# Performance work log

Hardware: AMD Instinct MI355X
Metric: run time of the kernel (lower is better)

Reference implementation:

```python
import math
import jax, jax.numpy as jnp
import numpy as np

H = 2048      # hidden_size
NH = 16       # num_attention_heads
QL = 1536     # q_lora_rank
KVL = 512     # kv_lora_rank
NOPE = 128    # qk_nope_head_dim
ROPE = 64     # qk_rope_head_dim
VD = 128      # v_head_dim
QKH = NOPE + ROPE
B, S = 2, 2048
EPS = 1e-6
MIN_VAL = -1e15


def _rms_norm(x, w, eps=EPS):
    var = jnp.mean(x * x, axis=-1, keepdims=True)
    return w * (x * jax.lax.rsqrt(var + eps))


def _rotate_half(x):
    x1, x2 = jnp.split(x, 2, axis=-1)
    return jnp.concatenate((-x2, x1), axis=-1)


def _rope_tables(seq_len, dim):
    inv_freq = 1.0 / (10000.0 ** (np.arange(0, dim, 2, dtype=np.float32) / dim))
    t = np.arange(seq_len, dtype=np.float32)[:, None]
    freqs = t @ inv_freq[None, :]
    freqs = np.concatenate((freqs, freqs), axis=-1)  # [S, dim]
    return jnp.asarray(np.cos(freqs)), jnp.asarray(np.sin(freqs))


def setup_inputs() -> dict:
    key = jax.random.key(0)
    ks = jax.random.split(key, 16)
    s = 0.02
    inp = {
        "x": jax.random.normal(ks[0], (B, S, H), dtype=jnp.float32),
        "mask": jnp.ones((B, S), dtype=jnp.int32),
        "wq_a_w": jax.random.normal(ks[1], (QL, H), dtype=jnp.float32) * s,
        "wq_a_b": jnp.zeros((QL,), dtype=jnp.float32),
        "q_norm_w": jnp.ones((QL,), dtype=jnp.float32),
        "wq_b_w": jax.random.normal(ks[2], (NH * QKH, QL), dtype=jnp.float32) * s,
        "wq_b_b": jnp.zeros((NH * QKH,), dtype=jnp.float32),
        "wkv_a_w": jax.random.normal(ks[3], (KVL + ROPE, H), dtype=jnp.float32) * s,
        "wkv_a_b": jnp.zeros((KVL + ROPE,), dtype=jnp.float32),
        "kv_norm_w": jnp.ones((KVL,), dtype=jnp.float32),
        "wkv_b_w": jax.random.normal(ks[4], (NH * (NOPE + VD), KVL), dtype=jnp.float32) * s,
        "wo_w": jax.random.normal(ks[5], (H, NH * VD), dtype=jnp.float32) * s,
        "wo_b": jnp.zeros((H,), dtype=jnp.float32),
    }
    return inp


def reference(x, mask, wq_a_w, wq_a_b, q_norm_w, wq_b_w, wq_b_b,
              wkv_a_w, wkv_a_b, kv_norm_w, wkv_b_w, wo_w, wo_b):
    bs, seq, _ = x.shape
    # ---- low-rank Q path ----
    q = x @ wq_a_w.T + wq_a_b                 # [b,s,QL]
    q = _rms_norm(q, q_norm_w)
    q = q @ wq_b_w.T + wq_b_b                 # [b,s,NH*QKH]
    q = q.reshape(bs, seq, NH, QKH)
    q_nope, q_pe = q[..., :NOPE], q[..., NOPE:]
    # ---- low-rank KV path ----
    kv_full = x @ wkv_a_w.T + wkv_a_b          # [b,s,KVL+ROPE]
    kv, k_pe = kv_full[..., :KVL], kv_full[..., KVL:]
    kv = _rms_norm(kv, kv_norm_w)              # latent kv cache [b,s,KVL]
    # ---- RoPE on the small rope slice only ----
    cos, sin = _rope_tables(seq, ROPE)         # [s,ROPE]
    cos_q, sin_q = cos[None, :, None, :], sin[None, :, None, :]
    q_pe = q_pe * cos_q + _rotate_half(q_pe) * sin_q            # [b,s,NH,ROPE]
    k_pe = k_pe * cos[None, :, :] + _rotate_half(k_pe) * sin[None, :, :]  # [b,s,ROPE]
    # ---- weight absorption ----
    wkv_b = wkv_b_w.reshape(NH, NOPE + VD, KVL)
    q_lat = jnp.einsum('bshd,hdc->bshc', q_nope, wkv_b[:, :NOPE])  # absorb W_UK
    scores = (jnp.einsum('bshc,btc->bsht', q_lat, kv)
              + jnp.einsum('bshr,btr->bsht', q_pe, k_pe)) / math.sqrt(QKH)
    # ---- causal + padding mask ----
    causal = jnp.triu(jnp.full((seq, seq), MIN_VAL, dtype=scores.dtype), k=1)
    m = jnp.where(mask[:, None, :] == 0, MIN_VAL, causal[None])    # [b,s,t]
    scores = scores + m[:, :, None, :]
    attn = jax.nn.softmax(scores, axis=-1)                         # [b,s,h,t]
    out = jnp.einsum('bsht,btc->bshc', attn, kv)                   # latent values
    out = jnp.einsum('bshc,hdc->bshd', out, wkv_b[:, NOPE:])       # absorb W_UV
    out = out.reshape(bs, seq, NH * VD) @ wo_w.T + wo_b
    return out
```

## Files before the change

kernel.cpp:

```cpp
#include <hip/hip_runtime.h>
#include <hip/hip_bf16.h>

#define BB   2
#define SS   2048
#define HH   2048
#define NHH  16
#define QLL  1536
#define KVLL 512
#define NOPE_D 128
#define ROPE_D 64
#define QKH_D  192
#define VD_D   128
#define MROWS  (BB*SS)

typedef __attribute__((ext_vector_type(8))) short bf16x8;
typedef __attribute__((ext_vector_type(4))) float f32x4;

__device__ inline float bf2f(unsigned short u) {
    union { float f; unsigned int i; } v; v.i = ((unsigned int)u) << 16; return v.f;
}
__device__ inline unsigned short f2bf(float f) {
    union { float f; unsigned int u; } v; v.f = f;
    unsigned int r = v.u + 0x7fffu + ((v.u >> 16) & 1u);
    return (unsigned short)(r >> 16);
}

__device__ __forceinline__ void gload_lds16(const ushort* g, ushort* l)
{
    __builtin_amdgcn_global_load_lds(
        (const __attribute__((address_space(1))) void*)(g),
        (__attribute__((address_space(3))) void*)(l), 16, 0, 0);
}

__global__ void conv_bf(const float* __restrict__ in, ushort* __restrict__ out, int n4)
{
    int i = blockIdx.x * 256 + threadIdx.x;
    int stride = gridDim.x * 256;
    for (; i < n4; i += stride) {
        float4 v = ((const float4*)in)[i];
        ushort4 u;
        u.x = f2bf(v.x); u.y = f2bf(v.y); u.z = f2bf(v.z); u.w = f2bf(v.w);
        ((ushort4*)out)[i] = u;
    }
}

template<typename TC>
__launch_bounds__(256, 3)
__global__ void gemm_bf(const ushort* __restrict__ A, int lda, size_t Ab, size_t Ah,
                        const ushort* __restrict__ B, int ldb, size_t Bb, size_t Bh,
                        const float* __restrict__ bias,
                        TC* __restrict__ C, int ldc, size_t Cb, size_t Ch,
                        int M, int N, int K)
{
    __shared__ ushort As[128 * 64];
    __shared__ ushort Bs[128 * 64];
    const int z = blockIdx.z, bz = z >> 4, hz = z & 15;
    A += (size_t)bz * Ab + (size_t)hz * Ah;
    B += (size_t)bz * Bb + (size_t)hz * Bh;
    C += (size_t)bz * Cb + (size_t)hz * Ch;
    const int m0 = blockIdx.y * 128, n0 = blockIdx.x * 128;
    const int tid = threadIdx.x, w = tid >> 6, lane = tid & 63;
    const int l15 = lane & 15, q = lane >> 4;
    const int r7 = lane >> 3, c7 = lane & 7;
    const int xork = l15 & 7;

    f32x4 acc[4][4];
#pragma unroll
    for (int i = 0; i < 4; i++)
#pragma unroll
        for (int j = 0; j < 4; j++) acc[i][j] = (f32x4){0.f, 0.f, 0.f, 0.f};

    const int mrow = 64 * (w & 1) + l15;
    const int nrow = 64 * (w >> 1) + l15;

    for (int k0 = 0; k0 < K; k0 += 64) {
#pragma unroll
        for (int i = 0; i < 4; i++) {
            int g = 4 * w + i;
            int row = g * 8 + r7;
            int ch = c7 ^ r7;
            gload_lds16(A + (size_t)(m0 + row) * lda + k0 + ch * 8,
                        As + g * 512 + lane * 8);
            int rb = n0 + row; if (rb > N - 1) rb = N - 1;
            gload_lds16(B + (size_t)rb * ldb + k0 + ch * 8,
                        Bs + g * 512 + lane * 8);
        }
        __syncthreads();
#pragma unroll
        for (int ks = 0; ks < 2; ks++) {
            bf16x8 af[4], bf[4];
            const int ch = ks * 4 + q, chx = ch ^ xork;
#pragma unroll
            for (int mt = 0; mt < 4; mt++)
                af[mt] = *(const bf16x8*)(As + (mrow + 16 * mt) * 64 + chx * 8);
#pragma unroll
            for (int nt = 0; nt < 4; nt++)
                bf[nt] = *(const bf16x8*)(Bs + (nrow + 16 * nt) * 64 + chx * 8);
#pragma unroll
            for (int mt = 0; mt < 4; mt++)
#pragma unroll
                for (int nt = 0; nt < 4; nt++)
                    acc[mt][nt] = __builtin_amdgcn_mfma_f32_16x16x32_bf16(af[mt], bf[nt], acc[mt][nt], 0, 0, 0);
        }
        __syncthreads();
    }

#pragma unroll
    for (int nt = 0; nt < 4; nt++) {
        int n = n0 + nrow + 16 * nt;
        if (n >= N) continue;
        float bv = bias ? bias[n] : 0.f;
#pragma unroll
        for (int mt = 0; mt < 4; mt++) {
#pragma unroll
            for (int r = 0; r < 4; r++) {
                int m = m0 + 64 * (w & 1) + 16 * mt + 4 * q + r;
                float v = acc[mt][nt][r] + bv;
                if constexpr (sizeof(TC) == 2) C[(size_t)m * ldc + n] = f2bf(v);
                else                           C[(size_t)m * ldc + n] = v;
            }
        }
    }
}

__launch_bounds__(256)
__global__ void rmsnorm_bf(const float* __restrict__ x, const float* __restrict__ w,
                           ushort* __restrict__ o, int width)
{
    const float* xr = x + (size_t)blockIdx.x * width;
    ushort* orow = o + (size_t)blockIdx.x * width;
    float ss = 0.f;
    for (int i = threadIdx.x; i < width; i += 256) { float v = xr[i]; ss += v * v; }
    __shared__ float red[256];
    red[threadIdx.x] = ss; __syncthreads();
    for (int off = 128; off > 0; off >>= 1) {
        if (threadIdx.x < off) red[threadIdx.x] += red[threadIdx.x + off];
        __syncthreads();
    }
    float r = rsqrtf(red[0] / (float)width + 1e-6f);
    for (int i = threadIdx.x; i < width; i += 256)
        orow[i] = f2bf(w[i] * xr[i] * r);
}

__device__ inline float rope_val(float xj, float xo, int j, int s)
{
    int i = j & 31;
    float freq = powf(10000.f, -(float)i / 32.f);
    float a = (float)s * freq;
    float sn, cs; sincosf(a, &sn, &cs);
    float other = (j < 32) ? -xo : xo;
    return xj * cs + other * sn;
}

__launch_bounds__(256)
__global__ void finalize_kv(const float* __restrict__ kvf, const float* __restrict__ w,
                            ushort* __restrict__ kvbf)
{
    int m = blockIdx.x, s = m & (SS - 1);
    const float* xr = kvf + (size_t)m * 576;
    float ss = 0.f;
    for (int i = threadIdx.x; i < 512; i += 256) { float v = xr[i]; ss += v * v; }
    __shared__ float red[256];
    red[threadIdx.x] = ss; __syncthreads();
    for (int off = 128; off > 0; off >>= 1) {
        if (threadIdx.x < off) red[threadIdx.x] += red[threadIdx.x + off];
        __syncthreads();
    }
    float r = rsqrtf(red[0] / 512.f + 1e-6f);
    for (int i = threadIdx.x; i < 512; i += 256)
        kvbf[(size_t)m * 576 + i] = f2bf(w[i] * xr[i] * r);
    if (threadIdx.x < 64) {
        int j = threadIdx.x;
        float xj = xr[512 + j], xo = xr[512 + (j ^ 32)];
        kvbf[(size_t)m * 576 + 512 + j] = f2bf(rope_val(xj, xo, j, s));
    }
}

__global__ void rope_q_kernel(ushort* __restrict__ qbuf)
{
    int m = blockIdx.x, s = m & (SS - 1);
    int w = threadIdx.x >> 6, j = threadIdx.x & 63;
    int h = blockIdx.y * 4 + w;
    ushort* p = qbuf + (size_t)m * 3072 + h * QKH_D + NOPE_D;
    float xj = bf2f(p[j]);
    float xo = bf2f(p[j ^ 32]);
    p[j] = f2bf(rope_val(xj, xo, j, s));
}

__global__ void copy_kpe(const ushort* __restrict__ kvbf, ushort* __restrict__ Kf)
{
    int m = blockIdx.x, b = m >> 11, t = m & (SS - 1);
    int j = threadIdx.x & 63;
    ushort v = kvbf[(size_t)m * 576 + 512 + j];
    for (int h = threadIdx.x >> 6; h < NHH; h += 4)
        Kf[((size_t)(b * NHH + h) * SS + t) * QKH_D + NOPE_D + j] = v;
}

#define SCL  0.10411760f
#define PTL  72
#define NJOB 45

__constant__ unsigned char JQT[NJOB] = {18,17,16,19,20,21,22,23,24,25,26,27,28,29,30,31,15,31,14,30,13,29,12,28,11,27,10,26,9,25,8,24,7,23,6,22,5,21,4,20,3,19,2,1,0};
__constant__ unsigned char JT0[NJOB] = { 0, 0, 0, 0, 0, 0, 0, 0, 0, 0, 0, 0, 0, 0, 0, 0, 0,16, 0,16, 0,16, 0,16, 0,16, 0,16, 0,16, 0,16, 0,16, 0,16, 0,16, 0,16, 0,16, 0, 0, 0};
__constant__ unsigned char JT1[NJOB] = {19,18,17,16,16,16,16,16,16,16,16,16,16,16,16,16,16,32,15,31,14,30,13,29,12,28,11,27,10,26, 9,25, 8,24, 7,23, 6,22, 5,21, 4,20, 3, 2, 1};

__device__ __forceinline__ int ktidx(int row, int ch) {
    return (((ch >> 3) << 3) + (row >> 3)) * 512 + (row & 7) * 64 + (((ch & 7) ^ (row & 7)) << 3);
}

__launch_bounds__(256, 4)
__global__ void attn_mfma(const ushort* __restrict__ qbuf, const ushort* __restrict__ Kf,
                          const ushort* __restrict__ VT, const int* __restrict__ mask,
                          ushort* __restrict__ o_heads,
                          ushort* __restrict__ Opart, float2* __restrict__ mlbuf)
{
    __shared__ ushort Kt[24 * 512];
    __shared__ ushort Pt[64 * PTL];
    __shared__ float alpha_sh[64];
    __shared__ float linv_sh[64];

    const int tid = threadIdx.x, w = tid >> 6, lane = tid & 63;
    const int l15 = lane & 15, q = lane >> 4;
    const int r7 = lane >> 3, c7 = lane & 7;

    const int job = blockIdx.x >> 5, bh = blockIdx.x & 31;
    const int b = bh >> 4, h = bh & 15;
    const int qt = JQT[job], t0s = JT0[job], t1s = JT1[job];
    const int s0 = qt * 64;
    const bool partial = (t0s != 0) | (t1s != qt + 1);

    const ushort* Kf_bh = Kf + (size_t)bh * SS * QKH_D;
    const ushort* VT_bh = VT + (size_t)bh * VD_D * SS;
    const int* mrow = mask + b * SS;

    bf16x8 qf[6];
    {
        const ushort* qbase = qbuf + ((size_t)(b * SS) + s0 + 16 * w + l15) * 3072 + h * QKH_D + q * 8;
#pragma unroll
        for (int k = 0; k < 6; k++) qf[k] = *(const bf16x8*)(qbase + k * 32);
    }

    f32x4 Oacc[2][4];
#pragma unroll
    for (int mt = 0; mt < 2; mt++)
#pragma unroll
        for (int nt = 0; nt < 4; nt++) Oacc[mt][nt] = (f32x4){0.f, 0.f, 0.f, 0.f};
    float m_i[4] = {-3e38f, -3e38f, -3e38f, -3e38f};
    float l_i[4] = {0.f, 0.f, 0.f, 0.f};

    for (int st = t0s; st < t1s; st++) {
        const int t0 = st * 64;
#pragma unroll
        for (int i = 0; i < 6; i++) {
            int g = 6 * w + i;
            int rg = g & 7, cg = g >> 3;
            int row = rg * 8 + r7;
            int ch = cg * 8 + (c7 ^ r7);
            gload_lds16(Kf_bh + (size_t)(t0 + row) * QKH_D + ch * 8,
                        Kt + g * 512 + lane * 8);
        }
        __syncthreads();
        f32x4 sa[4];
#pragma unroll
        for (int c = 0; c < 4; c++) sa[c] = (f32x4){0.f, 0.f, 0.f, 0.f};
#pragma unroll
        for (int k = 0; k < 6; k++) {
#pragma unroll
            for (int c = 0; c < 4; c++) {
                bf16x8 kb = *(const bf16x8*)(Kt + ktidx(16 * c + l15, 4 * k + q));
                sa[c] = __builtin_amdgcn_mfma_f32_16x16x32_bf16(qf[k], kb, sa[c], 0, 0, 0);
            }
        }
        int mv[4];
#pragma unroll
        for (int c = 0; c < 4; c++) mv[c] = mrow[t0 + 16 * c + l15];
        float alpha[4];
#pragma unroll
        for (int r = 0; r < 4; r++) {
            const int srow = s0 + 16 * w + 4 * q + r;
            float s_c[4];
#pragma unroll
            for (int c = 0; c < 4; c++) {
                s_c[c] = sa[c][r] * SCL;
                int col = t0 + 16 * c + l15;
                if (col > srow || mv[c] == 0) s_c[c] = -1e30f;
            }
            float mx = fmaxf(fmaxf(s_c[0], s_c[1]), fmaxf(s_c[2], s_c[3]));
            mx = fmaxf(mx, __shfl_xor(mx, 1)); mx = fmaxf(mx, __shfl_xor(mx, 2));
            mx = fmaxf(mx, __shfl_xor(mx, 4)); mx = fmaxf(mx, __shfl_xor(mx, 8));
            float mn = fmaxf(m_i[r], mx);
            alpha[r] = exp2f(m_i[r] - mn);
            m_i[r] = mn;
            float ps = 0.f;
            const int prow = 16 * w + 4 * q + r;
#pragma unroll
            for (int c = 0; c < 4; c++) {
                float pc = (s_c[c] <= -1e29f) ? 0.f : exp2f(s_c[c] - mn);
                ps += pc;
                Pt[prow * PTL + 16 * c + l15] = f2bf(pc);
            }
            ps += __shfl_xor(ps, 1); ps += __shfl_xor(ps, 2);
            ps += __shfl_xor(ps, 4); ps += __shfl_xor(ps, 8);
            l_i[r] = l_i[r] * alpha[r] + ps;
        }
        if (l15 == 0) {
#pragma unroll
            for (int r = 0; r < 4; r++) alpha_sh[16 * w + 4 * q + r] = alpha[r];
        }
        __syncthreads();
        float av[4];
#pragma unroll
        for (int nt = 0; nt < 4; nt++) av[nt] = alpha_sh[16 * nt + l15];
#pragma unroll
        for (int mt = 0; mt < 2; mt++)
#pragma unroll
            for (int nt = 0; nt < 4; nt++) {
                Oacc[mt][nt][0] *= av[nt]; Oacc[mt][nt][1] *= av[nt];
                Oacc[mt][nt][2] *= av[nt]; Oacc[mt][nt][3] *= av[nt];
            }
        bf16x8 pb[4][2];
#pragma unroll
        for (int nt = 0; nt < 4; nt++)
#pragma unroll
            for (int kt = 0; kt < 2; kt++)
                pb[nt][kt] = *(const bf16x8*)(Pt + (16 * nt + l15) * PTL + kt * 32 + q * 8);
#pragma unroll
        for (int mt = 0; mt < 2; mt++) {
#pragma unroll
            for (int kt = 0; kt < 2; kt++) {
                bf16x8 af = *(const bf16x8*)(VT_bh + (size_t)(32 * w + 16 * mt + l15) * SS + t0 + kt * 32 + q * 8);
#pragma unroll
                for (int nt = 0; nt < 4; nt++)
                    Oacc[mt][nt] = __builtin_amdgcn_mfma_f32_16x16x32_bf16(af, pb[nt][kt], Oacc[mt][nt], 0, 0, 0);
            }
        }
        __syncthreads();
    }

    if (l15 == 0) {
#pragma unroll
        for (int r = 0; r < 4; r++)
            linv_sh[16 * w + 4 * q + r] = (l_i[r] > 0.f) ? 1.f / l_i[r] : 0.f;
    }
    __syncthreads();

    if (!partial) {
#pragma unroll
        for (int mt = 0; mt < 2; mt++)
#pragma unroll
            for (int nt = 0; nt < 4; nt++) {
                float lv = linv_sh[16 * nt + l15];
                int s = s0 + 16 * nt + l15;
                int d = 32 * w + 16 * mt + 4 * q;
                ushort4 pk;
                pk.x = f2bf(Oacc[mt][nt][0] * lv); pk.y = f2bf(Oacc[mt][nt][1] * lv);
                pk.z = f2bf(Oacc[mt][nt][2] * lv); pk.w = f2bf(Oacc[mt][nt][3] * lv);
                *(ushort4*)(o_heads + (size_t)(b * SS + s) * 2048 + h * VD_D + d) = pk;
            }
    } else {
        const int sp = (t0s != 0);
        const int p = bh * 26 + (qt - 19) * 2 + sp;
#pragma unroll
        for (int mt = 0; mt < 2; mt++)
#pragma unroll
            for (int nt = 0; nt < 4; nt++) {
                float lv = linv_sh[16 * nt + l15];
                int rl = 16 * nt + l15;
                int d = 32 * w + 16 * mt + 4 * q;
                ushort4 pk;
                pk.x = f2bf(Oacc[mt][nt][0] * lv); pk.y = f2bf(Oacc[mt][nt][1] * lv);
                pk.z = f2bf(Oacc[mt][nt][2] * lv); pk.w = f2bf(Oacc[mt][nt][3] * lv);
                *(ushort4*)(Opart + ((size_t)p * 64 + rl) * 128 + d) = pk;
            }
        if (l15 == 0) {
#pragma unroll
            for (int r = 0; r < 4; r++)
                mlbuf[p * 64 + 16 * w + 4 * q + r] = make_float2(m_i[r], l_i[r]);
        }
    }
}

__launch_bounds__(256)
__global__ void attn_merge(const ushort* __restrict__ Opart, const float2* __restrict__ mlbuf,
                           ushort* __restrict__ o_heads)
{
    int bh = blockIdx.x & 31, qi = blockIdx.x >> 5;
    int b = bh >> 4, h = bh & 15;
    int qt = 19 + qi;
    int t = threadIdx.x;
    int row = t >> 2, dbase = (t & 3) * 32;
    int p0 = bh * 26 + qi * 2, p1 = p0 + 1;
    float2 ml0 = mlbuf[p0 * 64 + row], ml1 = mlbuf[p1 * 64 + row];
    float M = fmaxf(ml0.x, ml1.x);
    float w0 = (ml0.y > 0.f) ? exp2f(ml0.x - M) * ml0.y : 0.f;
    float w1 = (ml1.y > 0.f) ? exp2f(ml1.x - M) * ml1.y : 0.f;
    float den = w0 + w1;
    float inv = (den > 0.f) ? 1.f / den : 0.f;
    w0 *= inv; w1 *= inv;
    int s = qt * 64 + row;
    const ushort* O0 = Opart + ((size_t)p0 * 64 + row) * 128 + dbase;
    const ushort* O1 = Opart + ((size_t)p1 * 64 + row) * 128 + dbase;
    ushort* dst = o_heads + (size_t)(b * SS + s) * 2048 + h * VD_D + dbase;
#pragma unroll
    for (int c = 0; c < 32; c += 8) {
        bf16x8 a = *(const bf16x8*)(O0 + c);
        bf16x8 bb = *(const bf16x8*)(O1 + c);
        bf16x8 o;
#pragma unroll
        for (int j = 0; j < 8; j++)
            o[j] = (short)f2bf(w0 * bf2f((unsigned short)a[j]) + w1 * bf2f((unsigned short)bb[j]));
        *(bf16x8*)(dst + c) = o;
    }
}

extern "C" void kernel_launch(void* const* d_in, const int* in_sizes, int n_in,
                              void* d_out, int out_size, void* d_ws, size_t ws_size,
                              hipStream_t stream)
{
    const float* x        = (const float*)d_in[0];
    const int*   mask     = (const int*)d_in[1];
    const float* wq_a_w   = (const float*)d_in[2];
    const float* wq_a_b   = (const float*)d_in[3];
    const float* q_norm_w = (const float*)d_in[4];
    const float* wq_b_w   = (const float*)d_in[5];
    const float* wq_b_b   = (const float*)d_in[6];
    const float* wkv_a_w  = (const float*)d_in[7];
    const float* wkv_a_b  = (const float*)d_in[8];
    const float* kv_norm_w= (const float*)d_in[9];
    const float* wkv_b_w  = (const float*)d_in[10];
    const float* wo_w     = (const float*)d_in[11];
    const float* wo_b     = (const float*)d_in[12];
    float* out = (float*)d_out;

    char* W = (char*)d_ws;
    ushort* wq_a_bf = (ushort*)(W + 0);
    ushort* qbuf    = (ushort*)(W + 0);
    float*  q_a     = (float*)(W + 25165824);
    ushort* Kf      = (ushort*)(W + 25165824);
    ushort* x_bf    = (ushort*)(W + 50331648);
    ushort* VT      = (ushort*)(W + 50331648);
    ushort* q_a_bf  = (ushort*)(W + 67108864);
    float*  kvf     = (float*)(W + 67108864);
    ushort* o_heads = (ushort*)(W + 67108864);
    ushort* wq_b_bf = (ushort*)(W + 83886080);
    ushort* kvbf    = (ushort*)(W + 83886080);
    ushort* Opart   = (ushort*)(W + 83886080);
    ushort* wkv_b_bf= (ushort*)(W + 93323264);
    ushort* wo_bf   = (ushort*)(W + 97517568);
    ushort* wkv_a_bf= (ushort*)(W + 105906176);
    float2* mlbuf   = (float2*)(W + 105906176);

    conv_bf<<<2048, 256, 0, stream>>>(x, x_bf, MROWS * HH / 4);
    conv_bf<<<2048, 256, 0, stream>>>(wq_a_w, wq_a_bf, QLL * HH / 4);
    conv_bf<<<2048, 256, 0, stream>>>(wq_b_w, wq_b_bf, 3072 * QLL / 4);
    conv_bf<<<1024, 256, 0, stream>>>(wkv_a_w, wkv_a_bf, 576 * HH / 4);
    conv_bf<<<1024, 256, 0, stream>>>(wkv_b_w, wkv_b_bf, NHH * 256 * 512 / 4);
    conv_bf<<<2048, 256, 0, stream>>>(wo_w, wo_bf, HH * 2048 / 4);

    gemm_bf<float><<<dim3(QLL/128, MROWS/128, 1), 256, 0, stream>>>(
        x_bf, HH, 0, 0, wq_a_bf, HH, 0, 0, wq_a_b, q_a, QLL, 0, 0, MROWS, QLL, HH);
    rmsnorm_bf<<<MROWS, 256, 0, stream>>>(q_a, q_norm_w, q_a_bf, QLL);
    gemm_bf<ushort><<<dim3(3072/128, MROWS/128, 1), 256, 0, stream>>>(
        q_a_bf, QLL, 0, 0, wq_b_bf, QLL, 0, 0, wq_b_b, qbuf, 3072, 0, 0, MROWS, 3072, QLL);
    gemm_bf<float><<<dim3(5, MROWS/128, 1), 256, 0, stream>>>(
        x_bf, HH, 0, 0, wkv_a_bf, HH, 0, 0, wkv_a_b, kvf, 576, 0, 0, MROWS, 576, HH);
    finalize_kv<<<MROWS, 256, 0, stream>>>(kvf, kv_norm_w, kvbf);
    rope_q_kernel<<<dim3(MROWS, 4), 256, 0, stream>>>(qbuf);
    gemm_bf<ushort><<<dim3(1, SS/128, 32), 256, 0, stream>>>(
        kvbf, 576, (size_t)SS * 576, 0,
        wkv_b_bf, 512, 0, (size_t)256 * 512,
        nullptr, Kf, QKH_D, (size_t)NHH * SS * QKH_D, (size_t)SS * QKH_D,
        SS, NOPE_D, 512);
    copy_kpe<<<MROWS, 256, 0, stream>>>(kvbf, Kf);
    gemm_bf<ushort><<<dim3(SS/128, 1, 32), 256, 0, stream>>>(
        wkv_b_bf + (size_t)128 * 512, 512, 0, (size_t)256 * 512,
        kvbf, 576, (size_t)SS * 576, 0,
        nullptr, VT, SS, (size_t)NHH * VD_D * SS, (size_t)VD_D * SS,
        VD_D, SS, 512);
    attn_mfma<<<NJOB * 32, 256, 0, stream>>>(qbuf, Kf, VT, mask, o_heads, Opart, mlbuf);
    attn_merge<<<13 * 32, 256, 0, stream>>>(Opart, mlbuf, o_heads);
    gemm_bf<float><<<dim3(HH/128, MROWS/128, 1), 256, 0, stream>>>(
        o_heads, NHH * VD_D, 0, 0, wo_bf, NHH * VD_D, 0, 0, wo_b, out, HH, 0, 0,
        MROWS, HH, NHH * VD_D);
}
```

Measured before the change: 545.8 us.

## Fuse conversions, drop K-rope copy, bf16 intermediates, restructure attention PV per-wave

```diff
diff --git a/kernel.cpp b/kernel.cpp
--- a/kernel.cpp
+++ b/kernel.cpp
@@ -32,16 +32,21 @@
         (__attribute__((address_space(3))) void*)(l), 16, 0, 0);
 }
 
-__global__ void conv_bf(const float* __restrict__ in, ushort* __restrict__ out, int n4)
-{
-    int i = blockIdx.x * 256 + threadIdx.x;
-    int stride = gridDim.x * 256;
-    for (; i < n4; i += stride) {
-        float4 v = ((const float4*)in)[i];
-        ushort4 u;
-        u.x = f2bf(v.x); u.y = f2bf(v.y); u.z = f2bf(v.z); u.w = f2bf(v.w);
-        ((ushort4*)out)[i] = u;
-    }
+__global__ void conv6(const float* s0, ushort* d0, int n0,
+                      const float* s1, ushort* d1, int n1,
+                      const float* s2, ushort* d2, int n2,
+                      const float* s3, ushort* d3, int n3,
+                      const float* s4, ushort* d4, int n4,
+                      const float* s5, ushort* d5, int n5)
+{
+    const int st = gridDim.x * 256;
+    const int t0 = blockIdx.x * 256 + threadIdx.x;
+    for (int i = t0; i < n0; i += st) { float4 v = ((const float4*)s0)[i]; ushort4 u; u.x=f2bf(v.x);u.y=f2bf(v.y);u.z=f2bf(v.z);u.w=f2bf(v.w); ((ushort4*)d0)[i]=u; }
+    for (int i = t0; i < n1; i += st) { float4 v = ((const float4*)s1)[i]; ushort4 u; u.x=f2bf(v.x);u.y=f2bf(v.y);u.z=f2bf(v.z);u.w=f2bf(v.w); ((ushort4*)d1)[i]=u; }
+    for (int i = t0; i < n2; i += st) { float4 v = ((const float4*)s2)[i]; ushort4 u; u.x=f2bf(v.x);u.y=f2bf(v.y);u.z=f2bf(v.z);u.w=f2bf(v.w); ((ushort4*)d2)[i]=u; }
+    for (int i = t0; i < n3; i += st) { float4 v = ((const float4*)s3)[i]; ushort4 u; u.x=f2bf(v.x);u.y=f2bf(v.y);u.z=f2bf(v.z);u.w=f2bf(v.w); ((ushort4*)d3)[i]=u; }
+    for (int i = t0; i < n4; i += st) { float4 v = ((const float4*)s4)[i]; ushort4 u; u.x=f2bf(v.x);u.y=f2bf(v.y);u.z=f2bf(v.z);u.w=f2bf(v.w); ((ushort4*)d4)[i]=u; }
+    for (int i = t0; i < n5; i += st) { float4 v = ((const float4*)s5)[i]; ushort4 u; u.x=f2bf(v.x);u.y=f2bf(v.y);u.z=f2bf(v.z);u.w=f2bf(v.w); ((ushort4*)d5)[i]=u; }
 }
 
 template<typename TC>
@@ -89,7 +94,7 @@
 #pragma unroll
         for (int ks = 0; ks < 2; ks++) {
             bf16x8 af[4], bf[4];
-            const int ch = ks * 4 + q, chx = ch ^ xork;
+            const int chx = (ks * 4 + q) ^ xork;
 #pragma unroll
             for (int mt = 0; mt < 4; mt++)
                 af[mt] = *(const bf16x8*)(As + (mrow + 16 * mt) * 64 + chx * 8);
@@ -124,13 +129,11 @@
 }
 
 __launch_bounds__(256)
-__global__ void rmsnorm_bf(const float* __restrict__ x, const float* __restrict__ w,
-                           ushort* __restrict__ o, int width)
-{
-    const float* xr = x + (size_t)blockIdx.x * width;
-    ushort* orow = o + (size_t)blockIdx.x * width;
+__global__ void rmsnorm_bf16(ushort* __restrict__ x, const float* __restrict__ w, int width)
+{
+    ushort* xr = x + (size_t)blockIdx.x * width;
     float ss = 0.f;
-    for (int i = threadIdx.x; i < width; i += 256) { float v = xr[i]; ss += v * v; }
+    for (int i = threadIdx.x; i < width; i += 256) { float v = bf2f(xr[i]); ss += v * v; }
     __shared__ float red[256];
     red[threadIdx.x] = ss; __syncthreads();
     for (int off = 128; off > 0; off >>= 1) {
@@ -139,7 +142,7 @@
     }
     float r = rsqrtf(red[0] / (float)width + 1e-6f);
     for (int i = threadIdx.x; i < width; i += 256)
-        orow[i] = f2bf(w[i] * xr[i] * r);
+        xr[i] = f2bf(w[i] * bf2f(xr[i]) * r);
 }
 
 __device__ inline float rope_val(float xj, float xo, int j, int s)
@@ -153,13 +156,13 @@
 }
 
 __launch_bounds__(256)
-__global__ void finalize_kv(const float* __restrict__ kvf, const float* __restrict__ w,
+__global__ void finalize_kv(const ushort* __restrict__ kvf, const float* __restrict__ w,
                             ushort* __restrict__ kvbf)
 {
     int m = blockIdx.x, s = m & (SS - 1);
-    const float* xr = kvf + (size_t)m * 576;
+    const ushort* xr = kvf + (size_t)m * 576;
     float ss = 0.f;
-    for (int i = threadIdx.x; i < 512; i += 256) { float v = xr[i]; ss += v * v; }
+    for (int i = threadIdx.x; i < 512; i += 256) { float v = bf2f(xr[i]); ss += v * v; }
     __shared__ float red[256];
     red[threadIdx.x] = ss; __syncthreads();
     for (int off = 128; off > 0; off >>= 1) {
@@ -168,10 +171,10 @@
     }
     float r = rsqrtf(red[0] / 512.f + 1e-6f);
     for (int i = threadIdx.x; i < 512; i += 256)
-        kvbf[(size_t)m * 576 + i] = f2bf(w[i] * xr[i] * r);
+        kvbf[(size_t)m * 576 + i] = f2bf(w[i] * bf2f(xr[i]) * r);
     if (threadIdx.x < 64) {
         int j = threadIdx.x;
-        float xj = xr[512 + j], xo = xr[512 + (j ^ 32)];
+        float xj = bf2f(xr[512 + j]), xo = bf2f(xr[512 + (j ^ 32)]);
         kvbf[(size_t)m * 576 + 512 + j] = f2bf(rope_val(xj, xo, j, s));
     }
 }
@@ -187,15 +190,6 @@
     p[j] = f2bf(rope_val(xj, xo, j, s));
 }
 
-__global__ void copy_kpe(const ushort* __restrict__ kvbf, ushort* __restrict__ Kf)
-{
-    int m = blockIdx.x, b = m >> 11, t = m & (SS - 1);
-    int j = threadIdx.x & 63;
-    ushort v = kvbf[(size_t)m * 576 + 512 + j];
-    for (int h = threadIdx.x >> 6; h < NHH; h += 4)
-        Kf[((size_t)(b * NHH + h) * SS + t) * QKH_D + NOPE_D + j] = v;
-}
-
 #define SCL  0.10411760f
 #define PTL  72
 #define NJOB 45
@@ -210,14 +204,12 @@
 
 __launch_bounds__(256, 4)
 __global__ void attn_mfma(const ushort* __restrict__ qbuf, const ushort* __restrict__ Kf,
-                          const ushort* __restrict__ VT, const int* __restrict__ mask,
-                          ushort* __restrict__ o_heads,
+                          const ushort* __restrict__ kvbf, const ushort* __restrict__ VT,
+                          const int* __restrict__ mask, ushort* __restrict__ o_heads,
                           ushort* __restrict__ Opart, float2* __restrict__ mlbuf)
 {
     __shared__ ushort Kt[24 * 512];
-    __shared__ ushort Pt[64 * PTL];
-    __shared__ float alpha_sh[64];
-    __shared__ float linv_sh[64];
+    __shared__ ushort Pt[4 * 16 * PTL];
 
     const int tid = threadIdx.x, w = tid >> 6, lane = tid & 63;
     const int l15 = lane & 15, q = lane >> 4;
@@ -229,9 +221,11 @@
     const int s0 = qt * 64;
     const bool partial = (t0s != 0) | (t1s != qt + 1);
 
-    const ushort* Kf_bh = Kf + (size_t)bh * SS * QKH_D;
+    const ushort* Kf_bh = Kf + (size_t)bh * SS * NOPE_D;
     const ushort* VT_bh = VT + (size_t)bh * VD_D * SS;
+    const ushort* kpe_b = kvbf + (size_t)b * SS * 576 + 512;
     const int* mrow = mask + b * SS;
+    ushort* Ptw = Pt + w * 16 * PTL;
 
     bf16x8 qf[6];
     {
@@ -240,11 +234,9 @@
         for (int k = 0; k < 6; k++) qf[k] = *(const bf16x8*)(qbase + k * 32);
     }
 
-    f32x4 Oacc[2][4];
-#pragma unroll
-    for (int mt = 0; mt < 2; mt++)
-#pragma unroll
-        for (int nt = 0; nt < 4; nt++) Oacc[mt][nt] = (f32x4){0.f, 0.f, 0.f, 0.f};
+    f32x4 Oacc[8];
+#pragma unroll
+    for (int nt = 0; nt < 8; nt++) Oacc[nt] = (f32x4){0.f, 0.f, 0.f, 0.f};
     float m_i[4] = {-3e38f, -3e38f, -3e38f, -3e38f};
     float l_i[4] = {0.f, 0.f, 0.f, 0.f};
 
@@ -255,9 +247,11 @@
             int g = 6 * w + i;
             int rg = g & 7, cg = g >> 3;
             int row = rg * 8 + r7;
-            int ch = cg * 8 + (c7 ^ r7);
-            gload_lds16(Kf_bh + (size_t)(t0 + row) * QKH_D + ch * 8,
-                        Kt + g * 512 + lane * 8);
+            int chl = c7 ^ r7;
+            const ushort* src = (cg < 2)
+                ? Kf_bh + (size_t)(t0 + row) * NOPE_D + (cg * 8 + chl) * 8
+                : kpe_b + (size_t)(t0 + row) * 576 + chl * 8;
+            gload_lds16(src, Kt + g * 512 + lane * 8);
         }
         __syncthreads();
         f32x4 sa[4];
@@ -292,86 +286,62 @@
             alpha[r] = exp2f(m_i[r] - mn);
             m_i[r] = mn;
             float ps = 0.f;
-            const int prow = 16 * w + 4 * q + r;
 #pragma unroll
             for (int c = 0; c < 4; c++) {
                 float pc = (s_c[c] <= -1e29f) ? 0.f : exp2f(s_c[c] - mn);
                 ps += pc;
-                Pt[prow * PTL + 16 * c + l15] = f2bf(pc);
+                Ptw[(4 * q + r) * PTL + 16 * c + l15] = f2bf(pc);
             }
             ps += __shfl_xor(ps, 1); ps += __shfl_xor(ps, 2);
             ps += __shfl_xor(ps, 4); ps += __shfl_xor(ps, 8);
             l_i[r] = l_i[r] * alpha[r] + ps;
         }
-        if (l15 == 0) {
-#pragma unroll
-            for (int r = 0; r < 4; r++) alpha_sh[16 * w + 4 * q + r] = alpha[r];
-        }
-        __syncthreads();
-        float av[4];
-#pragma unroll
-        for (int nt = 0; nt < 4; nt++) av[nt] = alpha_sh[16 * nt + l15];
-#pragma unroll
-        for (int mt = 0; mt < 2; mt++)
-#pragma unroll
-            for (int nt = 0; nt < 4; nt++) {
-                Oacc[mt][nt][0] *= av[nt]; Oacc[mt][nt][1] *= av[nt];
-                Oacc[mt][nt][2] *= av[nt]; Oacc[mt][nt][3] *= av[nt];
-            }
-        bf16x8 pb[4][2];
-#pragma unroll
-        for (int nt = 0; nt < 4; nt++)
-#pragma unroll
-            for (int kt = 0; kt < 2; kt++)
-                pb[nt][kt] = *(const bf16x8*)(Pt + (16 * nt + l15) * PTL + kt * 32 + q * 8);
-#pragma unroll
-        for (int mt = 0; mt < 2; mt++) {
-#pragma unroll
-            for (int kt = 0; kt < 2; kt++) {
-                bf16x8 af = *(const bf16x8*)(VT_bh + (size_t)(32 * w + 16 * mt + l15) * SS + t0 + kt * 32 + q * 8);
-#pragma unroll
-                for (int nt = 0; nt < 4; nt++)
-                    Oacc[mt][nt] = __builtin_amdgcn_mfma_f32_16x16x32_bf16(af, pb[nt][kt], Oacc[mt][nt], 0, 0, 0);
-            }
-        }
-        __syncthreads();
-    }
-
-    if (l15 == 0) {
-#pragma unroll
-        for (int r = 0; r < 4; r++)
-            linv_sh[16 * w + 4 * q + r] = (l_i[r] > 0.f) ? 1.f / l_i[r] : 0.f;
-    }
-    __syncthreads();
+#pragma unroll
+        for (int nt = 0; nt < 8; nt++) {
+            Oacc[nt][0] *= alpha[0]; Oacc[nt][1] *= alpha[1];
+            Oacc[nt][2] *= alpha[2]; Oacc[nt][3] *= alpha[3];
+        }
+        bf16x8 pa[2];
+#pragma unroll
+        for (int kt = 0; kt < 2; kt++)
+            pa[kt] = *(const bf16x8*)(Ptw + l15 * PTL + kt * 32 + q * 8);
+#pragma unroll
+        for (int nt = 0; nt < 8; nt++) {
+            const ushort* vb = VT_bh + (size_t)(16 * nt + l15) * SS + t0 + q * 8;
+            bf16x8 v0 = *(const bf16x8*)(vb);
+            bf16x8 v1 = *(const bf16x8*)(vb + 32);
+            Oacc[nt] = __builtin_amdgcn_mfma_f32_16x16x32_bf16(pa[0], v0, Oacc[nt], 0, 0, 0);
+            Oacc[nt] = __builtin_amdgcn_mfma_f32_16x16x32_bf16(pa[1], v1, Oacc[nt], 0, 0, 0);
+        }
+        __syncthreads();
+    }
+
+    float lv[4];
+#pragma unroll
+    for (int r = 0; r < 4; r++) lv[r] = (l_i[r] > 0.f) ? 1.f / l_i[r] : 0.f;
 
     if (!partial) {
 #pragma unroll
-        for (int mt = 0; mt < 2; mt++)
-#pragma unroll
-            for (int nt = 0; nt < 4; nt++) {
-                float lv = linv_sh[16 * nt + l15];
-                int s = s0 + 16 * nt + l15;
-                int d = 32 * w + 16 * mt + 4 * q;
-                ushort4 pk;
-                pk.x = f2bf(Oacc[mt][nt][0] * lv); pk.y = f2bf(Oacc[mt][nt][1] * lv);
-                pk.z = f2bf(Oacc[mt][nt][2] * lv); pk.w = f2bf(Oacc[mt][nt][3] * lv);
-                *(ushort4*)(o_heads + (size_t)(b * SS + s) * 2048 + h * VD_D + d) = pk;
-            }
+        for (int nt = 0; nt < 8; nt++) {
+            int d = 16 * nt + l15;
+#pragma unroll
+            for (int r = 0; r < 4; r++) {
+                int s = s0 + 16 * w + 4 * q + r;
+                o_heads[(size_t)(b * SS + s) * 2048 + h * VD_D + d] = f2bf(Oacc[nt][r] * lv[r]);
+            }
+        }
     } else {
         const int sp = (t0s != 0);
         const int p = bh * 26 + (qt - 19) * 2 + sp;
 #pragma unroll
-        for (int mt = 0; mt < 2; mt++)
-#pragma unroll
-            for (int nt = 0; nt < 4; nt++) {
-                float lv = linv_sh[16 * nt + l15];
-                int rl = 16 * nt + l15;
-                int d = 32 * w + 16 * mt + 4 * q;
-                ushort4 pk;
-                pk.x = f2bf(Oacc[mt][nt][0] * lv); pk.y = f2bf(Oacc[mt][nt][1] * lv);
-                pk.z = f2bf(Oacc[mt][nt][2] * lv); pk.w = f2bf(Oacc[mt][nt][3] * lv);
-                *(ushort4*)(Opart + ((size_t)p * 64 + rl) * 128 + d) = pk;
-            }
+        for (int nt = 0; nt < 8; nt++) {
+            int d = 16 * nt + l15;
+#pragma unroll
+            for (int r = 0; r < 4; r++) {
+                int rl = 16 * w + 4 * q + r;
+                Opart[((size_t)p * 64 + rl) * 128 + d] = f2bf(Oacc[nt][r] * lv[r]);
+            }
+        }
         if (l15 == 0) {
 #pragma unroll
             for (int r = 0; r < 4; r++)
@@ -433,51 +403,50 @@
     float* out = (float*)d_out;
 
     char* W = (char*)d_ws;
-    ushort* wq_a_bf = (ushort*)(W + 0);
-    ushort* qbuf    = (ushort*)(W + 0);
-    float*  q_a     = (float*)(W + 25165824);
-    ushort* Kf      = (ushort*)(W + 25165824);
-    ushort* x_bf    = (ushort*)(W + 50331648);
-    ushort* VT      = (ushort*)(W + 50331648);
-    ushort* q_a_bf  = (ushort*)(W + 67108864);
-    float*  kvf     = (float*)(W + 67108864);
-    ushort* o_heads = (ushort*)(W + 67108864);
-    ushort* wq_b_bf = (ushort*)(W + 83886080);
-    ushort* kvbf    = (ushort*)(W + 83886080);
-    ushort* Opart   = (ushort*)(W + 83886080);
-    ushort* wkv_b_bf= (ushort*)(W + 93323264);
-    ushort* wo_bf   = (ushort*)(W + 97517568);
-    ushort* wkv_a_bf= (ushort*)(W + 105906176);
-    float2* mlbuf   = (float2*)(W + 105906176);
-
-    conv_bf<<<2048, 256, 0, stream>>>(x, x_bf, MROWS * HH / 4);
-    conv_bf<<<2048, 256, 0, stream>>>(wq_a_w, wq_a_bf, QLL * HH / 4);
-    conv_bf<<<2048, 256, 0, stream>>>(wq_b_w, wq_b_bf, 3072 * QLL / 4);
-    conv_bf<<<1024, 256, 0, stream>>>(wkv_a_w, wkv_a_bf, 576 * HH / 4);
-    conv_bf<<<1024, 256, 0, stream>>>(wkv_b_w, wkv_b_bf, NHH * 256 * 512 / 4);
-    conv_bf<<<2048, 256, 0, stream>>>(wo_w, wo_bf, HH * 2048 / 4);
-
-    gemm_bf<float><<<dim3(QLL/128, MROWS/128, 1), 256, 0, stream>>>(
-        x_bf, HH, 0, 0, wq_a_bf, HH, 0, 0, wq_a_b, q_a, QLL, 0, 0, MROWS, QLL, HH);
-    rmsnorm_bf<<<MROWS, 256, 0, stream>>>(q_a, q_norm_w, q_a_bf, QLL);
+    ushort* wo_bf    = (ushort*)(W + 0);
+    ushort* qbuf     = (ushort*)(W + 8388608);
+    ushort* wq_b_bf  = (ushort*)(W + 33554432);
+    ushort* Kf       = (ushort*)(W + 33554432);
+    ushort* wq_a_bf  = (ushort*)(W + 42991616);
+    ushort* kvfull_bf= (ushort*)(W + 42991616);
+    ushort* x_bf     = (ushort*)(W + 50331648);
+    ushort* VT       = (ushort*)(W + 50331648);
+    ushort* q_a_bf   = (ushort*)(W + 67108864);
+    ushort* o_heads  = (ushort*)(W + 67108864);
+    ushort* wkv_a_bf = (ushort*)(W + 79691776);
+    ushort* wkv_b_bf = (ushort*)(W + 83886080);
+    ushort* Opart    = (ushort*)(W + 83886080);
+    float2* mlbuf    = (float2*)(W + 97517568);
+    ushort* kvbf     = (ushort*)(W + 97943552);
+
+    conv6<<<4096, 256, 0, stream>>>(
+        x, x_bf, MROWS * HH / 4,
+        wq_a_w, wq_a_bf, QLL * HH / 4,
+        wq_b_w, wq_b_bf, 3072 * QLL / 4,
+        wkv_a_w, wkv_a_bf, 576 * HH / 4,
+        wkv_b_w, wkv_b_bf, NHH * 256 * 512 / 4,
+        wo_w, wo_bf, HH * 2048 / 4);
+
+    gemm_bf<ushort><<<dim3(QLL/128, MROWS/128, 1), 256, 0, stream>>>(
+        x_bf, HH, 0, 0, wq_a_bf, HH, 0, 0, wq_a_b, q_a_bf, QLL, 0, 0, MROWS, QLL, HH);
+    rmsnorm_bf16<<<MROWS, 256, 0, stream>>>(q_a_bf, q_norm_w, QLL);
     gemm_bf<ushort><<<dim3(3072/128, MROWS/128, 1), 256, 0, stream>>>(
         q_a_bf, QLL, 0, 0, wq_b_bf, QLL, 0, 0, wq_b_b, qbuf, 3072, 0, 0, MROWS, 3072, QLL);
-    gemm_bf<float><<<dim3(5, MROWS/128, 1), 256, 0, stream>>>(
-        x_bf, HH, 0, 0, wkv_a_bf, HH, 0, 0, wkv_a_b, kvf, 576, 0, 0, MROWS, 576, HH);
-    finalize_kv<<<MROWS, 256, 0, stream>>>(kvf, kv_norm_w, kvbf);
+    gemm_bf<ushort><<<dim3(5, MROWS/128, 1), 256, 0, stream>>>(
+        x_bf, HH, 0, 0, wkv_a_bf, HH, 0, 0, wkv_a_b, kvfull_bf, 576, 0, 0, MROWS, 576, HH);
+    finalize_kv<<<MROWS, 256, 0, stream>>>(kvfull_bf, kv_norm_w, kvbf);
     rope_q_kernel<<<dim3(MROWS, 4), 256, 0, stream>>>(qbuf);
     gemm_bf<ushort><<<dim3(1, SS/128, 32), 256, 0, stream>>>(
         kvbf, 576, (size_t)SS * 576, 0,
         wkv_b_bf, 512, 0, (size_t)256 * 512,
-        nullptr, Kf, QKH_D, (size_t)NHH * SS * QKH_D, (size_t)SS * QKH_D,
+        nullptr, Kf, NOPE_D, (size_t)NHH * SS * NOPE_D, (size_t)SS * NOPE_D,
         SS, NOPE_D, 512);
-    copy_kpe<<<MROWS, 256, 0, stream>>>(kvbf, Kf);
     gemm_bf<ushort><<<dim3(SS/128, 1, 32), 256, 0, stream>>>(
         wkv_b_bf + (size_t)128 * 512, 512, 0, (size_t)256 * 512,
         kvbf, 576, (size_t)SS * 576, 0,
         nullptr, VT, SS, (size_t)NHH * VD_D * SS, (size_t)VD_D * SS,
         VD_D, SS, 512);
-    attn_mfma<<<NJOB * 32, 256, 0, stream>>>(qbuf, Kf, VT, mask, o_heads, Opart, mlbuf);
+    attn_mfma<<<NJOB * 32, 256, 0, stream>>>(qbuf, Kf, kvbf, VT, mask, o_heads, Opart, mlbuf);
     attn_merge<<<13 * 32, 256, 0, stream>>>(Opart, mlbuf, o_heads);
     gemm_bf<float><<<dim3(HH/128, MROWS/128, 1), 256, 0, stream>>>(
         o_heads, NHH * VD_D, 0, 0, wo_bf, NHH * VD_D, 0, 0, wo_b, out, HH, 0, 0,
```

Result: slower. 607.1 us (+11.2%).
